# Performance work log

Measured on AMD Instinct MI355X. Metric: run time of the kernel, lower is better.

The kernel has to match this reference:

```python
import jax, jax.numpy as jnp
import numpy as np

B, L, D, F, K, M = 32, 1024, 384, 384, 3, 4096
LN_EPS = 1e-5


def setup_inputs() -> dict:
    key = jax.random.key(0)
    ks = jax.random.split(key, 6)
    w = lambda k, shp: jax.random.normal(k, shp, jnp.float32) * 0.02
    return {
        "x": jax.random.normal(ks[0], (B, L, D), jnp.float32),
        "target": jax.random.randint(ks[1], (B, L), 0, 5),
        "mel_max_length": M,
        "conv1_w": w(ks[2], (F, D, K)),  # OIW layout
        "conv1_b": jnp.zeros((F,), jnp.float32),
        "ln1_g": jnp.ones((F,), jnp.float32),
        "ln1_b": jnp.zeros((F,), jnp.float32),
        "conv2_w": w(ks[3], (F, F, K)),
        "conv2_b": jnp.zeros((F,), jnp.float32),
        "ln2_g": jnp.ones((F,), jnp.float32),
        "ln2_b": jnp.zeros((F,), jnp.float32),
        "lin_w": w(ks[4], (F, 1)),
        "lin_b": jnp.zeros((1,), jnp.float32),
    }


def conv1d_same(x, w, b):
    # x: [B, L, C], w: [O, I, K] -> [B, L, O], 'same' padding
    pad = (w.shape[-1] - 1) // 2
    y = jax.lax.conv_general_dilated(
        x, w, window_strides=(1,), padding=[(pad, pad)],
        dimension_numbers=("NWC", "OIW", "NWC"))
    return y + b


def layernorm(x, g, b):
    m = jnp.mean(x, axis=-1, keepdims=True)
    v = jnp.mean(jnp.square(x - m), axis=-1, keepdims=True)
    return (x - m) * jax.lax.rsqrt(v + LN_EPS) * g + b


def duration_predictor(x, c1w, c1b, g1, b1, c2w, c2b, g2, b2, lw, lb):
    h = jnp.maximum(layernorm(conv1d_same(x, c1w, c1b), g1, b1), 0.0)
    h = jnp.maximum(layernorm(conv1d_same(h, c2w, c2b), g2, b2), 0.0)
    return jnp.maximum(h @ lw + lb, 0.0)[..., 0]  # [B, L]


def length_regulate(x, durations, mel_max_length):
    # Equivalent to one-hot alignment matmul + zero pad, done as a gather.
    cum = jnp.cumsum(durations, axis=1)  # [B, L]
    t = jnp.arange(mel_max_length)       # [M]
    # frame t belongs to phoneme j where cum[j-1] <= t < cum[j]
    idx = jax.vmap(lambda c: jnp.searchsorted(c, t, side="right"))(cum)  # [B, M]
    valid = (t[None, :] < cum[:, -1:]).astype(x.dtype)                    # [B, M]
    idx = jnp.minimum(idx, durations.shape[1] - 1)
    out = jnp.take_along_axis(x, idx[..., None], axis=1) * valid[..., None]
    return out  # [B, M, D]


def reference(x, target, mel_max_length, conv1_w, conv1_b, ln1_g, ln1_b,
              conv2_w, conv2_b, ln2_g, ln2_b, lin_w, lin_b):
    dur_pred = duration_predictor(x, conv1_w, conv1_b, ln1_g, ln1_b,
                                  conv2_w, conv2_b, ln2_g, ln2_b, lin_w, lin_b)
    out = length_regulate(x, target, mel_max_length)
    return out, dur_pred
```

## Files before the change

kernel.cpp:

```cpp
#include <hip/hip_runtime.h>

#define DEV __device__ __forceinline__

typedef unsigned short u16;
typedef __attribute__((ext_vector_type(8))) short bf16x8;
typedef __attribute__((ext_vector_type(8))) unsigned short u16x8;
typedef __attribute__((ext_vector_type(4))) float f32x4;

constexpr int Bz = 32, Lz = 1024, Dz = 384, Fz = 384, KWz = 3, Mz = 4096;
constexpr float EPS = 1e-5f;

DEV u16 f2bf(float f) {
  unsigned u = __float_as_uint(f);
  u += 0x7fffu + ((u >> 16) & 1u);
  return (u16)(u >> 16);
}

typedef __attribute__((address_space(1))) const unsigned char ga_t;
typedef __attribute__((address_space(3))) unsigned char la_t;
DEV void gload16(const void* g, void* l) {
  __builtin_amdgcn_global_load_lds((ga_t*)g, (la_t*)l, 16, 0, 0);
}

#define WAITV(n) asm volatile("s_waitcnt vmcnt(" #n ")" ::: "memory")

__global__ __launch_bounds__(1024) void k_pre(
    const float* __restrict__ w1, const float* __restrict__ w2,
    u16* __restrict__ w1t, u16* __restrict__ w2t, u16* __restrict__ h1,
    const int* __restrict__ tgt, int* __restrict__ idxb) {
  __shared__ int sc[Lz];
  constexpr int WT = KWz * Fz * Dz;
  constexpr int PREP_ELEMS = 2 * WT + Bz * 2 * Dz;
  constexpr int PREP_BLKS = (PREP_ELEMS + 1023) / 1024;
  const int tid = threadIdx.x;

  if (blockIdx.x < PREP_BLKS) {
    int gid = blockIdx.x * 1024 + tid;
    if (gid < WT) {
      int k = gid / (Fz * Dz), rem = gid % (Fz * Dz);
      int f = rem / Dz, d = rem % Dz;
      w1t[gid] = f2bf(w1[(f * Dz + d) * KWz + k]);
    } else if (gid < 2 * WT) {
      int g2 = gid - WT;
      int k = g2 / (Fz * Fz), rem = g2 % (Fz * Fz);
      int co = rem / Fz, ci = rem % Fz;
      w2t[g2] = f2bf(w2[(co * Fz + ci) * KWz + k]);
    } else if (gid < PREP_ELEMS) {
      int p = gid - 2 * WT;
      int b = p / (2 * Dz), r = (p / Dz) & 1, d = p % Dz;
      size_t row = (size_t)b * (Lz + 2) + (r ? (Lz + 1) : 0);
      h1[row * Dz + d] = 0;
    }
    return;
  }
  int b = blockIdx.x - PREP_BLKS;
  sc[tid] = tgt[b * Lz + tid];
  __syncthreads();
  for (int off = 1; off < Lz; off <<= 1) {
    int add = (tid >= off) ? sc[tid - off] : 0;
    __syncthreads();
    sc[tid] += add;
    __syncthreads();
  }
  int total = sc[Lz - 1];
  for (int t = tid; t < Mz; t += 1024) {
    int lo = 0, hi = Lz;
    while (lo < hi) {
      int mid = (lo + hi) >> 1;
      if (sc[mid] > t) hi = mid; else lo = mid + 1;
    }
    int iv = (t < total) ? (lo > Lz - 1 ? Lz - 1 : lo) : -1;
    idxb[b * Mz + t] = iv;
  }
}

__global__ void k_gather(const float* __restrict__ x, const int* __restrict__ idxb,
                         float* __restrict__ out) {
  int wid = (blockIdx.x * blockDim.x + threadIdx.x) >> 6;
  int lane = threadIdx.x & 63;
  int nw = (gridDim.x * blockDim.x) >> 6;
  for (int row = wid; row < Bz * Mz; row += nw) {
    int b = row >> 12;
    int iv = idxb[row];
    float4* dst = reinterpret_cast<float4*>(out + (size_t)row * Dz);
    if (iv < 0) {
      float4 z = make_float4(0.f, 0.f, 0.f, 0.f);
      dst[lane] = z;
      if (lane < 32) dst[64 + lane] = z;
    } else {
      const float4* src =
          reinterpret_cast<const float4*>(x + ((size_t)b * Lz + iv) * Dz);
      dst[lane] = src[lane];
      if (lane < 32) dst[64 + lane] = src[64 + lane];
    }
  }
}

template <int LAYER>
__global__ __launch_bounds__(512, 2) void k_conv(
    const void* __restrict__ Asrc,
    const u16* __restrict__ wt,
    const float* __restrict__ cbias,
    const float* __restrict__ lng, const float* __restrict__ lnb,
    u16* __restrict__ hout,
    const float* __restrict__ lw, const float* __restrict__ lbias,
    float* __restrict__ dur)
{
  constexpr int ABUFS = (LAYER == 1) ? 2 : 3;
  __shared__ __align__(16) u16 Ash[ABUFS][8192];
  __shared__ __align__(16) u16 Bsh[3][384 * 32];
  __shared__ float s_sum[4][128], s_sq[4][128], s_dot[4][128];

  const int tid = threadIdx.x;
  const int lane = tid & 63, wave = tid >> 6;
  const int wr = wave >> 2, wc = wave & 3;
  const int l15 = lane & 15, lh = lane >> 4;
  const int b = blockIdx.x >> 3, l0 = (blockIdx.x & 7) << 7;
  const bf16x8 zfrag = {0, 0, 0, 0, 0, 0, 0, 0};

  int bgof[3], bldo[3];
  #pragma unroll
  for (int i = 0; i < 3; ++i) {
    int c = wave + 8 * i;
    int slot = c * 64 + lane, f = slot >> 2, q = slot & 3;
    int ks = q ^ ((f >> 1) & 3);
    bgof[i] = f * 384 + ks * 8;
    bldo[i] = c * 512;
  }
  auto STAGE_B = [&](int kt) {
    int tap = kt % 3, dw = kt / 3;
    const u16* sb = wt + tap * (384 * 384) + dw * 32;
    u16* dst = Bsh[tap];
    #pragma unroll
    for (int i = 0; i < 3; ++i) gload16(sb + bgof[i], dst + bldo[i]);
  };

  const float* arow_ptr = nullptr;
  const u16* a2src[2] = {nullptr, nullptr};
  int a2ldo[2] = {0, 0};
  float4 ar0, ar1, ar2, ar3;
  if constexpr (LAYER == 1) {
    int r1 = tid & 255, g1 = tid >> 8;
    int grow = l0 - 1 + r1;
    if (grow > l0 + 135) grow = l0 + 135;
    if (grow < 0) grow = 0;
    if (grow > Lz - 1) grow = Lz - 1;
    arow_ptr = (const float*)Asrc + (size_t)b * Lz * 384 + (size_t)grow * 384 +
               g1 * 8;
  } else {
    #pragma unroll
    for (int i = 0; i < 2; ++i) {
      int c = wave + 8 * i;
      int s = c * 64 + lane, g = s >> 8, r = s & 255;
      int p = l0 + r;
      if (p > l0 + 135) p = l0 + 135;
      if (p > Lz + 1) p = Lz + 1;
      a2src[i] = (const u16*)Asrc + (size_t)b * (Lz + 2) * 384 +
                 (size_t)p * 384 + g * 8;
      a2ldo[i] = c * 512;
    }
  }
  auto AISSUE = [&](int w) {
    const float* p = arow_ptr + w * 32;
    ar0 = *reinterpret_cast<const float4*>(p);
    ar1 = *reinterpret_cast<const float4*>(p + 4);
    ar2 = *reinterpret_cast<const float4*>(p + 16);
    ar3 = *reinterpret_cast<const float4*>(p + 20);
  };
  auto ADSW = [&](int wbuf) {
    u16x8 h0, h1;
    h0[0] = f2bf(ar0.x); h0[1] = f2bf(ar0.y); h0[2] = f2bf(ar0.z); h0[3] = f2bf(ar0.w);
    h0[4] = f2bf(ar1.x); h0[5] = f2bf(ar1.y); h0[6] = f2bf(ar1.z); h0[7] = f2bf(ar1.w);
    h1[0] = f2bf(ar2.x); h1[1] = f2bf(ar2.y); h1[2] = f2bf(ar2.z); h1[3] = f2bf(ar2.w);
    h1[4] = f2bf(ar3.x); h1[5] = f2bf(ar3.y); h1[6] = f2bf(ar3.z); h1[7] = f2bf(ar3.w);
    *reinterpret_cast<u16x8*>(&Ash[wbuf][tid * 8]) = h0;
    *reinterpret_cast<u16x8*>(&Ash[wbuf][(tid + 512) * 8]) = h1;
  };
  auto STAGE_A2 = [&](int w, int buf) {
    #pragma unroll
    for (int i = 0; i < 2; ++i) gload16(a2src[i] + w * 32, &Ash[buf][a2ldo[i]]);
  };

  int tr[4], boff[6];
  #pragma unroll
  for (int m = 0; m < 4; ++m) tr[m] = wr * 64 + m * 16 + l15;
  #pragma unroll
  for (int n = 0; n < 6; ++n) {
    int c = wc * 96 + n * 16 + l15;
    boff[n] = c * 32 + (lh ^ ((c >> 1) & 3)) * 8;
  }

  f32x4 acc[4][6] = {};

  if constexpr (LAYER == 1) {
    AISSUE(0);
    WAITV(0);
    ADSW(0);
    AISSUE(1);
    __builtin_amdgcn_sched_barrier(0);
    STAGE_B(0);
    STAGE_B(1);
  } else {
    STAGE_A2(0, 0);
    STAGE_B(0);
    STAGE_A2(1, 1);
    STAGE_B(1);
  }

#define PHASE(T)                                                               \
  {                                                                            \
    if constexpr ((T) == 0) {                                                  \
      if constexpr (LAYER == 2) {                                              \
        if (w == 0) { WAITV(5); } else { WAITV(3); }                           \
      } else { WAITV(3); }                                                     \
    } else if constexpr ((T) == 1) {                                           \
      if (w <= 9) {                                                            \
        if constexpr (LAYER == 1) { WAITV(7); } else { WAITV(5); }             \
      } else { WAITV(3); }                                                     \
    } else {                                                                   \
      if (w <= 9) {                                                            \
        if constexpr (LAYER == 1) { WAITV(7); } else { WAITV(5); }             \
      } else if (w == 10) { WAITV(3); } else { WAITV(0); }                     \
    }                                                                          \
    asm volatile("s_waitcnt lgkmcnt(0)" ::: "memory");                         \
    __builtin_amdgcn_s_barrier();                                              \
    __builtin_amdgcn_sched_barrier(0);                                         \
    const int abuf_ = (LAYER == 1) ? (w & 1) : (w % 3);                        \
    bf16x8 av[4], bv[6];                                                       \
    _Pragma("unroll")                                                          \
    for (int m = 0; m < 4; ++m) {                                              \
      av[m] = *reinterpret_cast<const bf16x8*>(                                \
          &Ash[abuf_][(lh * 256 + tr[m] + (T)) * 8]);                          \
      if constexpr (LAYER == 1 && (T) != 1) {                                  \
        int gr = l0 + tr[m] + (T) - 1;                                         \
        if ((unsigned)gr > (unsigned)(Lz - 1)) av[m] = zfrag;                  \
      }                                                                        \
    }                                                                          \
    _Pragma("unroll")                                                          \
    for (int n = 0; n < 6; ++n)                                                \
      bv[n] = *reinterpret_cast<const bf16x8*>(&Bsh[(T)][boff[n]]);            \
    __builtin_amdgcn_sched_barrier(0);                                         \
    { int kt2_ = 3 * w + (T) + 2; if (kt2_ <= 35) STAGE_B(kt2_); }             \
    __builtin_amdgcn_sched_barrier(0);                                         \
    if constexpr (LAYER == 1 && (T) == 0) {                                    \
      if (w <= 10) ADSW((w + 1) & 1);       \
    }                                                                          \
    if constexpr ((T) == 0) {                                                  \
      if (w <= 9) {                                                            \
        if constexpr (LAYER == 1) { AISSUE(w + 2); }                           \
        else { STAGE_A2(w + 2, (w + 2) % 3); }                                 \
      }                                                                        \
    }                                                                          \
    __builtin_amdgcn_sched_barrier(0);                                         \
    __builtin_amdgcn_s_setprio(1);                                             \
    _Pragma("unroll")                                                          \
    for (int m = 0; m < 4; ++m)                                                \
      _Pragma("unroll")                                                        \
      for (int n = 0; n < 6; ++n)                                              \
        acc[m][n] = __builtin_amdgcn_mfma_f32_16x16x32_bf16(av[m], bv[n],      \
                                                            acc[m][n], 0, 0, 0);\
    __builtin_amdgcn_s_setprio(0);                                             \
  }

  for (int w = 0; w < 12; ++w) {
    PHASE(0)
    PHASE(1)
    PHASE(2)
  }
#undef PHASE

  __syncthreads();
  float gv[6], bvv[6], cbv[6], lwv[6];
  #pragma unroll
  for (int n = 0; n < 6; ++n) {
    int c = wc * 96 + n * 16 + l15;
    gv[n] = lng[c]; bvv[n] = lnb[c]; cbv[n] = cbias[c];
    lwv[n] = (LAYER == 2) ? lw[c] : 0.f;
  }
  #pragma unroll
  for (int m = 0; m < 4; ++m) {
    #pragma unroll
    for (int r = 0; r < 4; ++r) {
      float s = 0.f, q2 = 0.f;
      #pragma unroll
      for (int n = 0; n < 6; ++n) {
        float v = acc[m][n][r] + cbv[n];
        s += v; q2 += v * v;
      }
      #pragma unroll
      for (int off = 1; off < 16; off <<= 1) {
        s += __shfl_xor(s, off);
        q2 += __shfl_xor(q2, off);
      }
      if (l15 == 0) {
        int row = wr * 64 + m * 16 + lh * 4 + r;
        s_sum[wc][row] = s;
        s_sq[wc][row] = q2;
      }
    }
  }
  __syncthreads();
  #pragma unroll
  for (int m = 0; m < 4; ++m) {
    #pragma unroll
    for (int r = 0; r < 4; ++r) {
      int row = wr * 64 + m * 16 + lh * 4 + r;
      float S = 0.f, Q = 0.f;
      #pragma unroll
      for (int w = 0; w < 4; ++w) { S += s_sum[w][row]; Q += s_sq[w][row]; }
      float mean = S * (1.f / 384.f);
      float var = Q * (1.f / 384.f) - mean * mean;
      float rstd = rsqrtf(var + EPS);
      float dotp = 0.f;
      #pragma unroll
      for (int n = 0; n < 6; ++n) {
        float v = acc[m][n][r] + cbv[n];
        float y = fmaxf((v - mean) * rstd * gv[n] + bvv[n], 0.f);
        if constexpr (LAYER == 1) {
          int c = wc * 96 + n * 16 + l15;
          hout[((size_t)(b * (Lz + 2) + l0 + row + 1)) * 384 + c] = f2bf(y);
        } else {
          dotp += y * lwv[n];
        }
      }
      if constexpr (LAYER == 2) {
        #pragma unroll
        for (int off = 1; off < 16; off <<= 1) dotp += __shfl_xor(dotp, off);
        if (l15 == 0) s_dot[wc][row] = dotp;
      }
    }
  }
  if constexpr (LAYER == 2) {
    __syncthreads();
    if (tid < 128) {
      float dsum = lbias[0];
      #pragma unroll
      for (int w = 0; w < 4; ++w) dsum += s_dot[w][tid];
      dur[(size_t)b * Lz + l0 + tid] = fmaxf(dsum, 0.f);
    }
  }
}

extern "C" void kernel_launch(void* const* d_in, const int* in_sizes, int n_in,
                              void* d_out, int out_size, void* d_ws, size_t ws_size,
                              hipStream_t stream) {
  (void)in_sizes; (void)n_in; (void)out_size; (void)ws_size;
  const float* x   = (const float*)d_in[0];
  const int* tgt   = (const int*)d_in[1];
  const float* w1  = (const float*)d_in[3];
  const float* c1b = (const float*)d_in[4];
  const float* g1  = (const float*)d_in[5];
  const float* b1  = (const float*)d_in[6];
  const float* w2  = (const float*)d_in[7];
  const float* c2b = (const float*)d_in[8];
  const float* g2  = (const float*)d_in[9];
  const float* b2  = (const float*)d_in[10];
  const float* lw  = (const float*)d_in[11];
  const float* lb  = (const float*)d_in[12];

  float* out0 = (float*)d_out;
  float* dur  = out0 + (size_t)Bz * Mz * Dz;

  const size_t h1_n = (size_t)Bz * (Lz + 2) * Dz;
  const size_t wt_n = (size_t)KWz * Fz * Dz;
  u16* h1  = (u16*)d_ws;
  u16* w1t = h1 + h1_n;
  u16* w2t = w1t + wt_n;
  int* idxb = (int*)(w2t + wt_n);

  constexpr int PREP_BLKS =
      (2 * KWz * Fz * Dz + Bz * 2 * Dz + 1023) / 1024;
  k_pre<<<PREP_BLKS + Bz, 1024, 0, stream>>>(w1, w2, w1t, w2t, h1, tgt, idxb);
  k_conv<1><<<256, 512, 0, stream>>>(x, w1t, c1b, g1, b1, h1, nullptr, nullptr,
                                     nullptr);
  k_conv<2><<<256, 512, 0, stream>>>(h1, w2t, c2b, g2, b2, nullptr, lw, lb, dur);
  k_gather<<<4096, 256, 0, stream>>>(x, idxb, out0);
}
```

Before: 120.9 us.

## Fuse length-regulator gather into conv kernels via extra producer waves

Removes the separate gather kernel and adds four extra waves per conv block (768 threads) that copy gathered rows of x into the output while the MFMA waves compute the convolution. Each conv launch handles half of the B*M rows, with a triple-buffered register pipeline and barrier counts matched to the compute waves' barriers. The aim is to overlap the memory-bound gather with the compute-bound convs and save a launch. In exchange, block size and register pressure rise, and the barrier counts must exactly match the hidden compute loop or the kernel will hang.

Result: slower. 212.8 us (+76.0%).

```diff
diff --git a/kernel.cpp b/kernel.cpp
--- a/kernel.cpp
+++ b/kernel.cpp
@@ -74,37 +74,18 @@
   }
 }
 
-__global__ void k_gather(const float* __restrict__ x, const int* __restrict__ idxb,
-                         float* __restrict__ out) {
-  int wid = (blockIdx.x * blockDim.x + threadIdx.x) >> 6;
-  int lane = threadIdx.x & 63;
-  int nw = (gridDim.x * blockDim.x) >> 6;
-  for (int row = wid; row < Bz * Mz; row += nw) {
-    int b = row >> 12;
-    int iv = idxb[row];
-    float4* dst = reinterpret_cast<float4*>(out + (size_t)row * Dz);
-    if (iv < 0) {
-      float4 z = make_float4(0.f, 0.f, 0.f, 0.f);
-      dst[lane] = z;
-      if (lane < 32) dst[64 + lane] = z;
-    } else {
-      const float4* src =
-          reinterpret_cast<const float4*>(x + ((size_t)b * Lz + iv) * Dz);
-      dst[lane] = src[lane];
-      if (lane < 32) dst[64 + lane] = src[64 + lane];
-    }
-  }
-}
-
 template <int LAYER>
-__global__ __launch_bounds__(512, 2) void k_conv(
+__global__ __launch_bounds__(768, 2) void k_conv(
     const void* __restrict__ Asrc,
     const u16* __restrict__ wt,
     const float* __restrict__ cbias,
     const float* __restrict__ lng, const float* __restrict__ lnb,
     u16* __restrict__ hout,
     const float* __restrict__ lw, const float* __restrict__ lbias,
-    float* __restrict__ dur)
+    float* __restrict__ dur,
+    const float* __restrict__ xf,
+    const int* __restrict__ idxb,
+    float* __restrict__ out0)
 {
   constexpr int ABUFS = (LAYER == 1) ? 2 : 3;
   __shared__ __align__(16) u16 Ash[ABUFS][8192];
@@ -113,10 +94,64 @@
 
   const int tid = threadIdx.x;
   const int lane = tid & 63, wave = tid >> 6;
-  const int wr = wave >> 2, wc = wave & 3;
   const int l15 = lane & 15, lh = lane >> 4;
   const int b = blockIdx.x >> 3, l0 = (blockIdx.x & 7) << 7;
   const bf16x8 zfrag = {0, 0, 0, 0, 0, 0, 0, 0};
+
+  if (wave >= 8) {
+    const int gw = wave - 8;
+    const int rbase = (LAYER == 1 ? 0 : (Bz * Mz) / 2) + blockIdx.x * 256 + gw * 64;
+    const int myidx = idxb[rbase + lane];
+
+    float4 A0[3], B0[3], A1[3], B1[3];
+
+    auto ldpair = [&](int p, float4& a0, float4& b0q, float4& a1, float4& b1q) {
+      int r0 = rbase + 2 * p;
+      int iv0 = __shfl(myidx, 2 * p), iv1 = __shfl(myidx, 2 * p + 1);
+      if (iv0 < 0) { a0 = make_float4(0.f, 0.f, 0.f, 0.f); b0q = a0; }
+      else {
+        const float4* s =
+            reinterpret_cast<const float4*>(xf + ((size_t)(r0 >> 12) * Lz + iv0) * Dz);
+        a0 = s[lane]; b0q = (lane < 32) ? s[64 + lane] : a0;
+      }
+      if (iv1 < 0) { a1 = make_float4(0.f, 0.f, 0.f, 0.f); b1q = a1; }
+      else {
+        const float4* s =
+            reinterpret_cast<const float4*>(xf + ((size_t)((r0 + 1) >> 12) * Lz + iv1) * Dz);
+        a1 = s[lane]; b1q = (lane < 32) ? s[64 + lane] : a1;
+      }
+    };
+    auto stpair = [&](int p, float4 a0, float4 b0q, float4 a1, float4 b1q) {
+      int r0 = rbase + 2 * p;
+      float4* d0 = reinterpret_cast<float4*>(out0 + (size_t)r0 * Dz);
+      d0[lane] = a0; if (lane < 32) d0[64 + lane] = b0q;
+      float4* d1 = reinterpret_cast<float4*>(out0 + (size_t)(r0 + 1) * Dz);
+      d1[lane] = a1; if (lane < 32) d1[64 + lane] = b1q;
+    };
+
+    ldpair(0, A0[0], B0[0], A1[0], B1[0]);
+    ldpair(1, A0[1], B0[1], A1[1], B1[1]);
+    for (int k3 = 0; k3 < 12; ++k3) {
+      int kt = 3 * k3;
+      if (kt < 30) ldpair(kt + 2, A0[2], B0[2], A1[2], B1[2]);
+      if (kt < 32) stpair(kt, A0[0], B0[0], A1[0], B1[0]);
+      __builtin_amdgcn_s_barrier();
+      ++kt;
+      if (kt < 30) ldpair(kt + 2, A0[0], B0[0], A1[0], B1[0]);
+      if (kt < 32) stpair(kt, A0[1], B0[1], A1[1], B1[1]);
+      __builtin_amdgcn_s_barrier();
+      ++kt;
+      if (kt < 30) ldpair(kt + 2, A0[1], B0[1], A1[1], B1[1]);
+      if (kt < 32) stpair(kt, A0[2], B0[2], A1[2], B1[2]);
+      __builtin_amdgcn_s_barrier();
+    }
+    __builtin_amdgcn_s_barrier();
+    __builtin_amdgcn_s_barrier();
+    if constexpr (LAYER == 2) __builtin_amdgcn_s_barrier();
+    return;
+  }
+
+  const int wr = wave >> 2, wc = wave & 3;
 
   int bgof[3], bldo[3];
   #pragma unroll
@@ -371,8 +406,8 @@
   constexpr int PREP_BLKS =
       (2 * KWz * Fz * Dz + Bz * 2 * Dz + 1023) / 1024;
   k_pre<<<PREP_BLKS + Bz, 1024, 0, stream>>>(w1, w2, w1t, w2t, h1, tgt, idxb);
-  k_conv<1><<<256, 512, 0, stream>>>(x, w1t, c1b, g1, b1, h1, nullptr, nullptr,
-                                     nullptr);
-  k_conv<2><<<256, 512, 0, stream>>>(h1, w2t, c2b, g2, b2, nullptr, lw, lb, dur);
-  k_gather<<<4096, 256, 0, stream>>>(x, idxb, out0);
+  k_conv<1><<<256, 768, 0, stream>>>(x, w1t, c1b, g1, b1, h1, nullptr, nullptr,
+                                     nullptr, x, idxb, out0);
+  k_conv<2><<<256, 768, 0, stream>>>(h1, w2t, c2b, g2, b2, nullptr, lw, lb, dur,
+                                     x, idxb, out0);
 }
```
